# Kernel tuning notes

Hardware: AMD Instinct MI355X
Metric: run time of the kernel (lower is better)

The kernel has to match this reference:

```python
import jax, jax.numpy as jnp
import numpy as np
import math

HORIZONS = (1, 5, 21)
TEMP = 0.07
N_NEG = 128
B, T, D = 16, 512, 256


def _normalize(x):
    # F.normalize(dim=-1): x / max(||x||, eps)
    return x / jnp.maximum(jnp.linalg.norm(x, axis=-1, keepdims=True), 1e-12)


def setup_inputs() -> dict:
    key = jax.random.key(0)
    k1, k2, k3 = jax.random.split(key, 3)
    z_seq = jax.random.normal(k1, (B, T, D), dtype=jnp.float32)
    # stacked per-horizon Linear weights (nn.Linear applies x @ W.T)
    preds = jax.random.normal(k2, (len(HORIZONS), D, D), dtype=jnp.float32) / np.float32(np.sqrt(D))
    neg_idx = jax.random.randint(k3, (len(HORIZONS), B * T, N_NEG), 0, B * T, dtype=jnp.int64)
    return {"z_seq": z_seq, "preds": preds, "neg_idx": neg_idx}


def reference(z_seq, preds, neg_idx):
    raw_w = {k: 1.0 / math.sqrt(k) for k in HORIZONS}
    tot_w = sum(raw_w.values())
    # detached, normalized pool of all timesteps used as negatives
    all_z = jax.lax.stop_gradient(_normalize(z_seq.reshape(B * T, D)))
    total = jnp.float32(0.0)
    for i, k in enumerate(HORIZONS):
        if k >= T:
            continue
        L = T - k
        # predictor: Linear without bias -> anchor @ W.T
        z_pred = jnp.einsum('bld,ed->ble', z_seq[:, :L, :], preds[i]).reshape(B * L, D)
        z_pred = _normalize(z_pred)
        z_pos = jax.lax.stop_gradient(_normalize(z_seq[:, k:, :].reshape(B * L, D)))
        idx = neg_idx[i, :B * L]                    # [B*L, N_NEG]
        z_neg = all_z[idx]                          # [B*L, N_NEG, D]
        pos_logit = jnp.sum(z_pred * z_pos, axis=-1, keepdims=True) / TEMP   # [B*L, 1]
        neg_logits = jnp.einsum('nkd,nd->nk', z_neg, z_pred) / TEMP          # [B*L, N_NEG]
        logits = jnp.concatenate([pos_logit, neg_logits], axis=1)
        # cross-entropy with label 0
        loss = jnp.mean(jax.nn.logsumexp(logits, axis=1) - logits[:, 0])
        total = total + jnp.float32(raw_w[k] / tot_w) * loss
    return total
```

## Files before the change

kernel.cpp:

```cpp
#include <hip/hip_runtime.h>
#include <math.h>

constexpr int Bc = 16, Tc = 512, Dc = 256, NNEGc = 128, BTc = Bc * Tc;
constexpr float TEMP_INV = 1.0f / 0.07f;
constexpr float QSCALE = TEMP_INV / (127.0f * 127.0f);
constexpr int GX = 2043;
constexpr int NPART = 3 * GX;

typedef __attribute__((ext_vector_type(8))) short short8;
typedef __attribute__((ext_vector_type(4))) float f32x4;
typedef __attribute__((ext_vector_type(4))) _Float16 f16x4;
typedef __attribute__((ext_vector_type(2))) _Float16 h2;

struct HP { int L, N, kh; float scale; long long nxOff; };
struct HP3 { HP h[3]; };

__device__ inline unsigned packh2(float a, float b) {
    h2 p = {(_Float16)a, (_Float16)b};
    return __builtin_bit_cast(unsigned, p);
}
__device__ inline float dot2(unsigned a, unsigned b, float c) {
#if __has_builtin(__builtin_amdgcn_fdot2)
    return __builtin_amdgcn_fdot2(__builtin_bit_cast(h2, a), __builtin_bit_cast(h2, b), c, false);
#else
    h2 x = __builtin_bit_cast(h2, a), y = __builtin_bit_cast(h2, b);
    return c + (float)x.x * (float)y.x + (float)x.y * (float)y.y;
#endif
}
__device__ inline int sdot4(unsigned a, unsigned b, int c) {
#if __has_builtin(__builtin_amdgcn_sdot4)
    return __builtin_amdgcn_sdot4((int)a, (int)b, c, false);
#else
    c += (int)(char)(a) * (int)(char)(b);
    c += (int)(char)(a >> 8) * (int)(char)(b >> 8);
    c += (int)(char)(a >> 16) * (int)(char)(b >> 16);
    c += (int)(char)(a >> 24) * (int)(char)(b >> 24);
    return c;
#endif
}
__device__ inline unsigned q4i8(float a, float b, float c, float d) {
    int qa = (int)rintf(a * 127.0f), qb = (int)rintf(b * 127.0f);
    int qc = (int)rintf(c * 127.0f), qd = (int)rintf(d * 127.0f);
    return (qa & 0xff) | ((qb & 0xff) << 8) | ((qc & 0xff) << 16) | ((unsigned)qd << 24);
}

__global__ __launch_bounds__(256) void k_norm(const float* __restrict__ z,
                                              const float* __restrict__ preds,
                                              unsigned* __restrict__ az,
                                              unsigned* __restrict__ ani,
                                              unsigned* __restrict__ Wh) {
    if (blockIdx.x < 96) {
        int base = blockIdx.x * 2048 + threadIdx.x * 8;
        float4 w0 = reinterpret_cast<const float4*>(preds + base)[0];
        float4 w1 = reinterpret_cast<const float4*>(preds + base)[1];
        uint4 o;
        o.x = packh2(w0.x, w0.y); o.y = packh2(w0.z, w0.w);
        o.z = packh2(w1.x, w1.y); o.w = packh2(w1.z, w1.w);
        reinterpret_cast<uint4*>(Wh)[blockIdx.x * 256 + threadIdx.x] = o;
    }
    int wid = threadIdx.x >> 6, lane = threadIdx.x & 63;
    int row = blockIdx.x * 4 + wid;
    float4 v = reinterpret_cast<const float4*>(z)[row * 64 + lane];
    float s = v.x * v.x + v.y * v.y + v.z * v.z + v.w * v.w;
#pragma unroll
    for (int off = 32; off; off >>= 1) s += __shfl_xor(s, off, 64);
    float inv = 1.0f / fmaxf(sqrtf(s), 1e-12f);
    float a = v.x * inv, b = v.y * inv, c = v.z * inv, d = v.w * inv;
    reinterpret_cast<uint2*>(az)[row * 64 + lane] = make_uint2(packh2(a, b), packh2(c, d));
    ani[row * 64 + lane] = q4i8(a, b, c, d);
}

__global__ __launch_bounds__(256) void k_gemm(const unsigned* __restrict__ az,
                                              const unsigned* __restrict__ Wh,
                                              _Float16* __restrict__ zp) {
    __shared__ uint4 As[2048];
    __shared__ uint4 Bs[2048];
    int wave = threadIdx.x >> 6, lane = threadIdx.x & 63;
    int t = threadIdx.x;
    int m0 = blockIdx.x * 64, g0 = blockIdx.y * 64;
    const uint4* A4 = reinterpret_cast<const uint4*>(az) + (size_t)m0 * 32;
    const uint4* B4 = reinterpret_cast<const uint4*>(Wh) + (size_t)g0 * 32;
#pragma unroll
    for (int i = 0; i < 8; ++i) {
        int f = i * 256 + t;
        int r = f >> 5, c = f & 31;
        int sw = r * 32 + ((c ^ r) & 31);
        As[sw] = A4[f];
        Bs[sw] = B4[f];
    }
    __syncthreads();
    int mrow = lane & 15, kq = lane >> 4;
    f32x4 acc[4] = {f32x4{0,0,0,0}, f32x4{0,0,0,0}, f32x4{0,0,0,0}, f32x4{0,0,0,0}};
    int arow = wave * 16 + mrow;
#pragma unroll
    for (int kb = 0; kb < 8; ++kb) {
        int col = kb * 4 + kq;
        uint4 ua = As[arow * 32 + ((col ^ arow) & 31)];
        short8 a = __builtin_bit_cast(short8, ua);
#pragma unroll
        for (int nt = 0; nt < 4; ++nt) {
            int brow = nt * 16 + mrow;
            uint4 ub = Bs[brow * 32 + ((col ^ brow) & 31)];
            acc[nt] = __builtin_amdgcn_mfma_f32_16x16x32_f16(
                a, __builtin_bit_cast(short8, ub), acc[nt], 0, 0, 0);
        }
    }
#pragma unroll
    for (int nt = 0; nt < 4; ++nt) {
        int g = g0 + nt * 16 + mrow;
        int h = g >> 8, e = g & 255;
        _Float16* dst = zp + ((size_t)h * BTc + m0 + wave * 16 + kq * 4) * Dc + e;
#pragma unroll
        for (int r = 0; r < 4; ++r) dst[(size_t)r * Dc] = (_Float16)acc[nt][r];
    }
}

__global__ __launch_bounds__(256, 4) void k_loss(const unsigned* __restrict__ az,
                                                 const unsigned* __restrict__ ani,
                                                 const _Float16* __restrict__ zp_base,
                                                 const int* __restrict__ nx_base,
                                                 float* __restrict__ partials,
                                                 HP3 P) {
    HP hp = P.h[blockIdx.y];
    __shared__ unsigned zq[4][64];
    __shared__ float partial[4];
    int wid = threadIdx.x >> 6, lane = threadIdx.x & 63;
    int q = lane >> 2, q4 = lane & 3;
    int n = blockIdx.x * 4 + wid;
    float contrib = 0.0f;
    if (n < hp.N) {
        int b = n / hp.L, l = n - b * hp.L;
        int row = b * Tc + l;
        f16x4 hv = reinterpret_cast<const f16x4*>(
                       zp_base + ((size_t)blockIdx.y * BTc + row) * Dc)[lane];
        float4 v = make_float4((float)hv.x, (float)hv.y, (float)hv.z, (float)hv.w);
        float s = v.x * v.x + v.y * v.y + v.z * v.z + v.w * v.w;
#pragma unroll
        for (int off = 32; off; off >>= 1) s += __shfl_xor(s, off, 64);
        float inv = 1.0f / fmaxf(sqrtf(s), 1e-12f);
        v.x *= inv; v.y *= inv; v.z *= inv; v.w *= inv;
        zq[wid][lane] = q4i8(v.x, v.y, v.z, v.w);
        unsigned u0 = packh2(v.x, v.y), u1 = packh2(v.z, v.w);
        uint2 pw = reinterpret_cast<const uint2*>(az + (size_t)(row + hp.kh) * 128)[lane];
        float pd = dot2(pw.y, u1, dot2(pw.x, u0, 0.0f));
#pragma unroll
        for (int off = 32; off; off >>= 1) pd += __shfl_xor(pd, off, 64);
        float pos = pd * TEMP_INV;
        const int* nx = nx_base + hp.nxOff + (size_t)n * NNEGc;
        int i1 = nx[lane], i2 = nx[lane + 64];
        int idxp[8];
#pragma unroll
        for (int p = 0; p < 8; ++p)
            idxp[p] = __shfl(p < 4 ? i1 : i2, (p & 3) * 16 + q, 64);
        uint4 zqv[4];
        const uint4* zl4 = reinterpret_cast<const uint4*>(zq[wid]);
#pragma unroll
        for (int c = 0; c < 4; ++c) zqv[c] = zl4[c * 4 + q4];
        const uint4* ni4 = reinterpret_cast<const uint4*>(ani);
        float lg[8];
#pragma unroll
        for (int p = 0; p < 8; ++p) {
            uint4 g0 = ni4[(size_t)idxp[p] * 16 + 0 * 4 + q4];
            uint4 g1 = ni4[(size_t)idxp[p] * 16 + 1 * 4 + q4];
            uint4 g2 = ni4[(size_t)idxp[p] * 16 + 2 * 4 + q4];
            uint4 g3 = ni4[(size_t)idxp[p] * 16 + 3 * 4 + q4];
            int acc = 0;
            acc = sdot4(g0.x, zqv[0].x, acc); acc = sdot4(g0.y, zqv[0].y, acc);
            acc = sdot4(g0.z, zqv[0].z, acc); acc = sdot4(g0.w, zqv[0].w, acc);
            acc = sdot4(g1.x, zqv[1].x, acc); acc = sdot4(g1.y, zqv[1].y, acc);
            acc = sdot4(g1.z, zqv[1].z, acc); acc = sdot4(g1.w, zqv[1].w, acc);
            acc = sdot4(g2.x, zqv[2].x, acc); acc = sdot4(g2.y, zqv[2].y, acc);
            acc = sdot4(g2.z, zqv[2].z, acc); acc = sdot4(g2.w, zqv[2].w, acc);
            acc = sdot4(g3.x, zqv[3].x, acc); acc = sdot4(g3.y, zqv[3].y, acc);
            acc = sdot4(g3.z, zqv[3].z, acc); acc = sdot4(g3.w, zqv[3].w, acc);
            acc += __shfl_xor(acc, 1, 64);
            acc += __shfl_xor(acc, 2, 64);
            lg[p] = (float)acc * QSCALE;
        }
        float mm = lg[0];
#pragma unroll
        for (int p = 1; p < 8; ++p) mm = fmaxf(mm, lg[p]);
#pragma unroll
        for (int off = 32; off; off >>= 1) mm = fmaxf(mm, __shfl_xor(mm, off, 64));
        mm = fmaxf(mm, pos);
        float sl = 0.0f;
#pragma unroll
        for (int p = 0; p < 8; ++p) sl += __expf(lg[p] - mm);
#pragma unroll
        for (int off = 32; off; off >>= 1) sl += __shfl_xor(sl, off, 64);
        float S = sl * 0.25f + __expf(pos - mm);
        contrib = (mm + __logf(S) - pos) * hp.scale;
    }
    if (lane == 0) partial[wid] = contrib;
    __syncthreads();
    if (threadIdx.x == 0)
        partials[blockIdx.y * GX + blockIdx.x] =
            partial[0] + partial[1] + partial[2] + partial[3];
}

__global__ __launch_bounds__(256) void k_final(const float* __restrict__ partials,
                                               float* __restrict__ out) {
    __shared__ float ws[4];
    int wid = threadIdx.x >> 6, lane = threadIdx.x & 63;
    float s = 0.0f;
    for (int i = threadIdx.x; i < NPART; i += 256) s += partials[i];
#pragma unroll
    for (int off = 32; off; off >>= 1) s += __shfl_xor(s, off, 64);
    if (lane == 0) ws[wid] = s;
    __syncthreads();
    if (threadIdx.x == 0) out[0] = ws[0] + ws[1] + ws[2] + ws[3];
}

extern "C" void kernel_launch(void* const* d_in, const int* in_sizes, int n_in,
                              void* d_out, int out_size, void* d_ws, size_t ws_size,
                              hipStream_t stream) {
    const float* z     = (const float*)d_in[0];
    const float* preds = (const float*)d_in[1];
    const int*   nidx  = (const int*)d_in[2];
    float* out = (float*)d_out;

    unsigned* az   = (unsigned*)d_ws;
    unsigned* ani  = (unsigned*)((char*)d_ws + (size_t)4194304);
    unsigned* Wh   = (unsigned*)((char*)d_ws + (size_t)6291456);
    _Float16* zp   = (_Float16*)((char*)d_ws + (size_t)6684672);
    float*    part = (float*)((char*)d_ws + (size_t)19267584);

    const int ks[3] = {1, 5, 21};
    double rw[3] = {1.0, 1.0 / sqrt(5.0), 1.0 / sqrt(21.0)};
    double tot = rw[0] + rw[1] + rw[2];

    HP3 P;
    for (int i = 0; i < 3; ++i) {
        int L = Tc - ks[i], N = Bc * L;
        P.h[i].L = L; P.h[i].N = N; P.h[i].kh = ks[i];
        P.h[i].scale = (float)(rw[i] / tot / (double)N);
        P.h[i].nxOff = (long long)i * BTc * NNEGc;
    }

    k_norm<<<BTc / 4, 256, 0, stream>>>(z, preds, az, ani, Wh);
    k_gemm<<<dim3(BTc / 64, (3 * Dc) / 64), 256, 0, stream>>>(az, Wh, zp);
    k_loss<<<dim3(GX, 3), 256, 0, stream>>>(az, ani, zp, nidx, part, P);
    k_final<<<1, 256, 0, stream>>>(part, out);
}
```

Measured before the change: 121.9 us.

## Double-buffer negative gathers, remap lanes to 16-lane groups, use fixed logsumexp max

Restructures the negative-logit loop so each 16-lane group handles one negative row (a full 256-byte int8 row per group), and double-buffers the gathered rows: the next four negatives are loaded while the current four are reduced. Negative index loads and the first gathers are issued before the anchor normalisation so their latency overlaps that math. The data-dependent max pass is replaced by the known bound 1/TEMP, since the logits are dot products of unit vectors, which removes two reductions. In exchange each negative needs four shuffle steps instead of two, register pressure rises from the buffers, and exp(x-1/T) can lose precision for small logits.

```diff
diff --git a/kernel.cpp b/kernel.cpp
--- a/kernel.cpp
+++ b/kernel.cpp
@@ -4,6 +4,7 @@
 constexpr int Bc = 16, Tc = 512, Dc = 256, NNEGc = 128, BTc = Bc * Tc;
 constexpr float TEMP_INV = 1.0f / 0.07f;
 constexpr float QSCALE = TEMP_INV / (127.0f * 127.0f);
+constexpr float FMAXL = TEMP_INV;
 constexpr int GX = 2043;
 constexpr int NPART = 3 * GX;
 
@@ -125,71 +126,69 @@
     __shared__ unsigned zq[4][64];
     __shared__ float partial[4];
     int wid = threadIdx.x >> 6, lane = threadIdx.x & 63;
-    int q = lane >> 2, q4 = lane & 3;
+    int g = lane >> 4, s = lane & 15;
     int n = blockIdx.x * 4 + wid;
     float contrib = 0.0f;
     if (n < hp.N) {
+        const int* nx = nx_base + hp.nxOff + (size_t)n * NNEGc;
+        int i1 = nx[lane], i2 = nx[lane + 64];
+        const uint4* ni4 = reinterpret_cast<const uint4*>(ani);
+#define IDX(p) __shfl(((p) < 16 ? i1 : i2), (((p) & 15) << 2) + g, 64)
+
         int b = n / hp.L, l = n - b * hp.L;
         int row = b * Tc + l;
         f16x4 hv = reinterpret_cast<const f16x4*>(
                        zp_base + ((size_t)blockIdx.y * BTc + row) * Dc)[lane];
+        uint2 pw = reinterpret_cast<const uint2*>(az + (size_t)(row + hp.kh) * 128)[lane];
+
+        uint4 buf[2][4];
+#pragma unroll
+        for (int j = 0; j < 4; ++j) buf[0][j] = ni4[(size_t)IDX(j) * 16 + s];
+
         float4 v = make_float4((float)hv.x, (float)hv.y, (float)hv.z, (float)hv.w);
-        float s = v.x * v.x + v.y * v.y + v.z * v.z + v.w * v.w;
-#pragma unroll
-        for (int off = 32; off; off >>= 1) s += __shfl_xor(s, off, 64);
-        float inv = 1.0f / fmaxf(sqrtf(s), 1e-12f);
+        float sq = v.x * v.x + v.y * v.y + v.z * v.z + v.w * v.w;
+#pragma unroll
+        for (int off = 32; off; off >>= 1) sq += __shfl_xor(sq, off, 64);
+        float inv = 1.0f / fmaxf(sqrtf(sq), 1e-12f);
         v.x *= inv; v.y *= inv; v.z *= inv; v.w *= inv;
         zq[wid][lane] = q4i8(v.x, v.y, v.z, v.w);
-        unsigned u0 = packh2(v.x, v.y), u1 = packh2(v.z, v.w);
-        uint2 pw = reinterpret_cast<const uint2*>(az + (size_t)(row + hp.kh) * 128)[lane];
-        float pd = dot2(pw.y, u1, dot2(pw.x, u0, 0.0f));
+        float pd = dot2(pw.y, packh2(v.z, v.w), dot2(pw.x, packh2(v.x, v.y), 0.0f));
 #pragma unroll
         for (int off = 32; off; off >>= 1) pd += __shfl_xor(pd, off, 64);
         float pos = pd * TEMP_INV;
-        const int* nx = nx_base + hp.nxOff + (size_t)n * NNEGc;
-        int i1 = nx[lane], i2 = nx[lane + 64];
-        int idxp[8];
-#pragma unroll
-        for (int p = 0; p < 8; ++p)
-            idxp[p] = __shfl(p < 4 ? i1 : i2, (p & 3) * 16 + q, 64);
-        uint4 zqv[4];
-        const uint4* zl4 = reinterpret_cast<const uint4*>(zq[wid]);
-#pragma unroll
-        for (int c = 0; c < 4; ++c) zqv[c] = zl4[c * 4 + q4];
-        const uint4* ni4 = reinterpret_cast<const uint4*>(ani);
-        float lg[8];
-#pragma unroll
-        for (int p = 0; p < 8; ++p) {
-            uint4 g0 = ni4[(size_t)idxp[p] * 16 + 0 * 4 + q4];
-            uint4 g1 = ni4[(size_t)idxp[p] * 16 + 1 * 4 + q4];
-            uint4 g2 = ni4[(size_t)idxp[p] * 16 + 2 * 4 + q4];
-            uint4 g3 = ni4[(size_t)idxp[p] * 16 + 3 * 4 + q4];
-            int acc = 0;
-            acc = sdot4(g0.x, zqv[0].x, acc); acc = sdot4(g0.y, zqv[0].y, acc);
-            acc = sdot4(g0.z, zqv[0].z, acc); acc = sdot4(g0.w, zqv[0].w, acc);
-            acc = sdot4(g1.x, zqv[1].x, acc); acc = sdot4(g1.y, zqv[1].y, acc);
-            acc = sdot4(g1.z, zqv[1].z, acc); acc = sdot4(g1.w, zqv[1].w, acc);
-            acc = sdot4(g2.x, zqv[2].x, acc); acc = sdot4(g2.y, zqv[2].y, acc);
-            acc = sdot4(g2.z, zqv[2].z, acc); acc = sdot4(g2.w, zqv[2].w, acc);
-            acc = sdot4(g3.x, zqv[3].x, acc); acc = sdot4(g3.y, zqv[3].y, acc);
-            acc = sdot4(g3.z, zqv[3].z, acc); acc = sdot4(g3.w, zqv[3].w, acc);
-            acc += __shfl_xor(acc, 1, 64);
-            acc += __shfl_xor(acc, 2, 64);
-            lg[p] = (float)acc * QSCALE;
+        uint4 zs = reinterpret_cast<const uint4*>(zq[wid])[s];
+
+        float sl = 0.0f;
+#pragma unroll
+        for (int k = 0; k < 8; ++k) {
+            int cur = k & 1, nxt = cur ^ 1;
+            if (k < 7) {
+#pragma unroll
+                for (int j = 0; j < 4; ++j) {
+                    int p = (k + 1) * 4 + j;
+                    buf[nxt][j] = ni4[(size_t)IDX(p) * 16 + s];
+                }
+            }
+#pragma unroll
+            for (int j = 0; j < 4; ++j) {
+                uint4 gl = buf[cur][j];
+                int acc = 0;
+                acc = sdot4(gl.x, zs.x, acc);
+                acc = sdot4(gl.y, zs.y, acc);
+                acc = sdot4(gl.z, zs.z, acc);
+                acc = sdot4(gl.w, zs.w, acc);
+                acc += __shfl_xor(acc, 1, 64);
+                acc += __shfl_xor(acc, 2, 64);
+                acc += __shfl_xor(acc, 4, 64);
+                acc += __shfl_xor(acc, 8, 64);
+                sl += __expf((float)acc * QSCALE - FMAXL);
+            }
         }
-        float mm = lg[0];
-#pragma unroll
-        for (int p = 1; p < 8; ++p) mm = fmaxf(mm, lg[p]);
-#pragma unroll
-        for (int off = 32; off; off >>= 1) mm = fmaxf(mm, __shfl_xor(mm, off, 64));
-        mm = fmaxf(mm, pos);
-        float sl = 0.0f;
-#pragma unroll
-        for (int p = 0; p < 8; ++p) sl += __expf(lg[p] - mm);
-#pragma unroll
-        for (int off = 32; off; off >>= 1) sl += __shfl_xor(sl, off, 64);
-        float S = sl * 0.25f + __expf(pos - mm);
-        contrib = (mm + __logf(S) - pos) * hp.scale;
+#undef IDX
+        sl += __shfl_xor(sl, 16, 64);
+        sl += __shfl_xor(sl, 32, 64);
+        float S = sl + __expf(pos - FMAXL);
+        contrib = (FMAXL + __logf(S) - pos) * hp.scale;
     }
     if (lane == 0) partial[wid] = contrib;
     __syncthreads();
```

After: 134.5 us. 10.3% more time.
